# Performance work log

Hardware: AMD Instinct MI355X
Metric: run time of the kernel (lower is better)

The kernel has to match this reference:

```python
import jax, jax.numpy as jnp
import numpy as np

B = 262144
N = 1_000_000
R = 64
H = 128


def setup_inputs() -> dict:
    key = jax.random.key(0)
    k1, k2, k3, k4, k5, k6 = jax.random.split(key, 6)
    return {
        "x": jax.random.randint(k1, (B,), 0, N),
        "y": jax.random.randint(k2, (B,), 0, N),
        "r": jax.random.randint(k3, (B,), 0, R),
        "l": jax.random.randint(k4, (B,), 0, 2),
        "Wx": jax.random.normal(k5, (N, H), dtype=jnp.float32),
        "Wr": jax.random.normal(k6, (R, H), dtype=jnp.float32),
    }


def reference(x, y, r, l, Wx, Wr):
    # one_hot(idx) @ W  ==  gather rows  (same math, no dense GEMM)
    embx = Wx[x]          # [B, H]
    emby = Wx[y]          # [B, H]
    embr = Wr[r]          # [B, H]

    # regulartion: sigmoid'(clamp(embr))
    s = jax.nn.sigmoid(jnp.clip(embr, -6.0, 6.0))
    re_embr = s * (1.0 - s)

    preds = jax.nn.sigmoid(jnp.sum(embx * emby * re_embr, axis=1))[:, None]  # [B,1]
    logits = jnp.concatenate([preds, 1.0 - preds], axis=1)                   # [B,2]

    # torch.nn.CrossEntropyLoss: mean(-log_softmax(logits)[i, l_i])
    log_probs = jax.nn.log_softmax(logits, axis=1)
    loss = -jnp.mean(jnp.take_along_axis(log_probs, l[:, None], axis=1))
    return logits, loss
```

## Files before the change

### kernel.cpp

```cpp
#include <hip/hip_runtime.h>
#include <math.h>


#define H_DIM 128

__global__ __launch_bounds__(256) void fused_kernel(
    const int* __restrict__ x, const int* __restrict__ y,
    const int* __restrict__ r, const int* __restrict__ l,
    const float* __restrict__ Wx, const float* __restrict__ Wr,
    float* __restrict__ logits, float* __restrict__ partials,
    int ngroups)
{
    const int group = threadIdx.x >> 5;
    const int lane  = threadIdx.x & 31;

    __shared__ float sloss[8];
    float lossacc = 0.0f;

    for (int g = blockIdx.x; g < ngroups; g += gridDim.x) {
        const int row = g * 8 + group;
        const int xi = x[row];
        const int yi = y[row];
        const int ri = r[row];
        const int li = l[row];

        const float4 a = *(const float4*)(Wx + (size_t)xi * H_DIM + lane * 4);
        const float4 b = *(const float4*)(Wx + (size_t)yi * H_DIM + lane * 4);
        const float4 w = *(const float4*)(Wr + (size_t)ri * H_DIM + lane * 4);

        float4 c;
        {
            float v0 = fminf(6.0f, fmaxf(-6.0f, w.x));
            float v1 = fminf(6.0f, fmaxf(-6.0f, w.y));
            float v2 = fminf(6.0f, fmaxf(-6.0f, w.z));
            float v3 = fminf(6.0f, fmaxf(-6.0f, w.w));
            float s0 = 1.0f / (1.0f + __expf(-v0));
            float s1 = 1.0f / (1.0f + __expf(-v1));
            float s2 = 1.0f / (1.0f + __expf(-v2));
            float s3 = 1.0f / (1.0f + __expf(-v3));
            c.x = s0 * (1.0f - s0);
            c.y = s1 * (1.0f - s1);
            c.z = s2 * (1.0f - s2);
            c.w = s3 * (1.0f - s3);
        }

        float d = a.x * b.x * c.x + a.y * b.y * c.y
                + a.z * b.z * c.z + a.w * b.w * c.w;
        #pragma unroll
        for (int off = 16; off > 0; off >>= 1) d += __shfl_xor(d, off, 64);

        if (lane == 0) {
            float p = 1.0f / (1.0f + __expf(-d));
            float q = 1.0f - p;
            *(float2*)(logits + (size_t)row * 2) = make_float2(p, q);
            float lse = __logf(__expf(p) + __expf(q));
            lossacc += lse - (li == 0 ? p : q);
        }
    }

    if (lane == 0) sloss[group] = lossacc;
    __syncthreads();
    if (threadIdx.x == 0) {
        float s = 0.0f;
        #pragma unroll
        for (int gi = 0; gi < 8; ++gi) s += sloss[gi];
        partials[blockIdx.x] = s;
    }
}

__global__ __launch_bounds__(256) void reduce_kernel(
    const float* __restrict__ partials, int n, float* __restrict__ out, double invB)
{
    __shared__ double sd[256];
    double acc = 0.0;
    for (int i = threadIdx.x; i < n; i += 256) acc += (double)partials[i];
    sd[threadIdx.x] = acc;
    __syncthreads();
    for (int s = 128; s > 0; s >>= 1) {
        if ((int)threadIdx.x < s) sd[threadIdx.x] += sd[threadIdx.x + s];
        __syncthreads();
    }
    if (threadIdx.x == 0) *out = (float)(sd[0] * invB);
}

extern "C" void kernel_launch(void* const* d_in, const int* in_sizes, int n_in,
                              void* d_out, int out_size, void* d_ws, size_t ws_size,
                              hipStream_t stream) {
    const int*   x  = (const int*)d_in[0];
    const int*   y  = (const int*)d_in[1];
    const int*   r  = (const int*)d_in[2];
    const int*   l  = (const int*)d_in[3];
    const float* Wx = (const float*)d_in[4];
    const float* Wr = (const float*)d_in[5];

    const int B = in_sizes[0];

    float* logits   = (float*)d_out;
    float* loss_out = logits + (size_t)B * 2;

    float* partials = (float*)d_ws;
    const int ngroups = (B + 7) / 8;
    const int NBLK = 4096;

    fused_kernel<<<NBLK, 256, 0, stream>>>(x, y, r, l, Wx, Wr, logits, partials, ngroups);
    reduce_kernel<<<1, 256, 0, stream>>>(partials, NBLK, loss_out, 1.0 / (double)B);
}
```

Before: 606.4 us.

## Stage indices in shared memory, process two rows per group, coalesce logits store

Replaces the grid-stride loop with one block per 32 rows. Each block first loads its x/y/r/l indices into shared memory with coalesced reads. Each 32-lane group then issues gathers for two rows at once, which puts more loads in flight per wavefront. Logits are staged in shared memory and written with one coalesced store per block. The cost is a much larger grid of 8192 blocks, and the reduce kernel now sums twice as many partials.

```diff
diff --git a/kernel.cpp b/kernel.cpp
--- a/kernel.cpp
+++ b/kernel.cpp
@@ -3,63 +3,101 @@
 
 
 #define H_DIM 128
+#define ROWS_PER_BLOCK 32
+
+__device__ __forceinline__ float4 reg4(float4 w) {
+    float4 c;
+    float v0 = fminf(6.0f, fmaxf(-6.0f, w.x));
+    float v1 = fminf(6.0f, fmaxf(-6.0f, w.y));
+    float v2 = fminf(6.0f, fmaxf(-6.0f, w.z));
+    float v3 = fminf(6.0f, fmaxf(-6.0f, w.w));
+    float s0 = 1.0f / (1.0f + __expf(-v0));
+    float s1 = 1.0f / (1.0f + __expf(-v1));
+    float s2 = 1.0f / (1.0f + __expf(-v2));
+    float s3 = 1.0f / (1.0f + __expf(-v3));
+    c.x = s0 * (1.0f - s0); c.y = s1 * (1.0f - s1);
+    c.z = s2 * (1.0f - s2); c.w = s3 * (1.0f - s3);
+    return c;
+}
+
+__device__ __forceinline__ float dot3(float4 a, float4 b, float4 c) {
+    return a.x * b.x * c.x + a.y * b.y * c.y + a.z * b.z * c.z + a.w * b.w * c.w;
+}
 
 __global__ __launch_bounds__(256) void fused_kernel(
     const int* __restrict__ x, const int* __restrict__ y,
     const int* __restrict__ r, const int* __restrict__ l,
     const float* __restrict__ Wx, const float* __restrict__ Wr,
-    float* __restrict__ logits, float* __restrict__ partials,
-    int ngroups)
+    float* __restrict__ logits, float* __restrict__ partials, int B)
 {
     const int group = threadIdx.x >> 5;
     const int lane  = threadIdx.x & 31;
+    const int base  = blockIdx.x * ROWS_PER_BLOCK;
 
+    __shared__ int   sx[ROWS_PER_BLOCK], sy[ROWS_PER_BLOCK], sr[ROWS_PER_BLOCK], sl[ROWS_PER_BLOCK];
+    __shared__ float slog[ROWS_PER_BLOCK * 2];
     __shared__ float sloss[8];
+
+    {
+        const int t = threadIdx.x;
+        if (t < 128) {
+            const int w = t >> 5, i = t & 31, gidx = base + i;
+            const bool ok = gidx < B;
+            if      (w == 0) sx[i] = ok ? x[gidx] : 0;
+            else if (w == 1) sy[i] = ok ? y[gidx] : 0;
+            else if (w == 2) sr[i] = ok ? r[gidx] : 0;
+            else             sl[i] = ok ? l[gidx] : 0;
+        }
+    }
+    __syncthreads();
+
     float lossacc = 0.0f;
+    const int nvalid = min(ROWS_PER_BLOCK, B - base);
 
-    for (int g = blockIdx.x; g < ngroups; g += gridDim.x) {
-        const int row = g * 8 + group;
-        const int xi = x[row];
-        const int yi = y[row];
-        const int ri = r[row];
-        const int li = l[row];
+    #pragma unroll
+    for (int s = 0; s < 4; s += 2) {
+        const int i0 = s * 8 + group;
+        const int i1 = i0 + 8;
 
-        const float4 a = *(const float4*)(Wx + (size_t)xi * H_DIM + lane * 4);
-        const float4 b = *(const float4*)(Wx + (size_t)yi * H_DIM + lane * 4);
-        const float4 w = *(const float4*)(Wr + (size_t)ri * H_DIM + lane * 4);
+        const int x0 = sx[i0], y0 = sy[i0], r0 = sr[i0];
+        const int x1 = sx[i1], y1 = sy[i1], r1 = sr[i1];
 
-        float4 c;
-        {
-            float v0 = fminf(6.0f, fmaxf(-6.0f, w.x));
-            float v1 = fminf(6.0f, fmaxf(-6.0f, w.y));
-            float v2 = fminf(6.0f, fmaxf(-6.0f, w.z));
-            float v3 = fminf(6.0f, fmaxf(-6.0f, w.w));
-            float s0 = 1.0f / (1.0f + __expf(-v0));
-            float s1 = 1.0f / (1.0f + __expf(-v1));
-            float s2 = 1.0f / (1.0f + __expf(-v2));
-            float s3 = 1.0f / (1.0f + __expf(-v3));
-            c.x = s0 * (1.0f - s0);
-            c.y = s1 * (1.0f - s1);
-            c.z = s2 * (1.0f - s2);
-            c.w = s3 * (1.0f - s3);
+        const float4 a0 = *(const float4*)(Wx + (size_t)x0 * H_DIM + lane * 4);
+        const float4 b0 = *(const float4*)(Wx + (size_t)y0 * H_DIM + lane * 4);
+        const float4 w0 = *(const float4*)(Wr + (size_t)r0 * H_DIM + lane * 4);
+        const float4 a1 = *(const float4*)(Wx + (size_t)x1 * H_DIM + lane * 4);
+        const float4 b1 = *(const float4*)(Wx + (size_t)y1 * H_DIM + lane * 4);
+        const float4 w1 = *(const float4*)(Wr + (size_t)r1 * H_DIM + lane * 4);
+
+        float d0 = dot3(a0, b0, reg4(w0));
+        float d1 = dot3(a1, b1, reg4(w1));
+        #pragma unroll
+        for (int off = 16; off > 0; off >>= 1) {
+            d0 += __shfl_xor(d0, off, 64);
+            d1 += __shfl_xor(d1, off, 64);
         }
 
-        float d = a.x * b.x * c.x + a.y * b.y * c.y
-                + a.z * b.z * c.z + a.w * b.w * c.w;
-        #pragma unroll
-        for (int off = 16; off > 0; off >>= 1) d += __shfl_xor(d, off, 64);
-
         if (lane == 0) {
-            float p = 1.0f / (1.0f + __expf(-d));
-            float q = 1.0f - p;
-            *(float2*)(logits + (size_t)row * 2) = make_float2(p, q);
-            float lse = __logf(__expf(p) + __expf(q));
-            lossacc += lse - (li == 0 ? p : q);
+            float p0 = 1.0f / (1.0f + __expf(-d0));
+            float p1 = 1.0f / (1.0f + __expf(-d1));
+            float q0 = 1.0f - p0, q1 = 1.0f - p1;
+            slog[i0 * 2] = p0; slog[i0 * 2 + 1] = q0;
+            slog[i1 * 2] = p1; slog[i1 * 2 + 1] = q1;
+            float lse0 = __logf(__expf(p0) + __expf(q0));
+            float lse1 = __logf(__expf(p1) + __expf(q1));
+            if (i0 < nvalid) lossacc += lse0 - (sl[i0] == 0 ? p0 : q0);
+            if (i1 < nvalid) lossacc += lse1 - (sl[i1] == 0 ? p1 : q1);
         }
     }
 
     if (lane == 0) sloss[group] = lossacc;
     __syncthreads();
+
+    {
+        const int t = threadIdx.x;
+        if (t < ROWS_PER_BLOCK * 2 && (base + (t >> 1)) < B)
+            logits[(size_t)base * 2 + t] = slog[t];
+    }
     if (threadIdx.x == 0) {
         float s = 0.0f;
         #pragma unroll
@@ -99,9 +137,8 @@
     float* loss_out = logits + (size_t)B * 2;
 
     float* partials = (float*)d_ws;
-    const int ngroups = (B + 7) / 8;
-    const int NBLK = 4096;
+    const int nblk = (B + ROWS_PER_BLOCK - 1) / ROWS_PER_BLOCK;
 
-    fused_kernel<<<NBLK, 256, 0, stream>>>(x, y, r, l, Wx, Wr, logits, partials, ngroups);
-    reduce_kernel<<<1, 256, 0, stream>>>(partials, NBLK, loss_out, 1.0 / (double)B);
+    fused_kernel<<<nblk, 256, 0, stream>>>(x, y, r, l, Wx, Wr, logits, partials, B);
+    reduce_kernel<<<1, 256, 0, stream>>>(partials, nblk, loss_out, 1.0 / (double)B);
 }
```

New measurement: 613.5 us. Within noise of the previous version (+1.2%).
